# Kernel tuning notes

Measured on AMD Instinct MI355X. Metric: run time of the kernel, lower is better.

The kernel has to match this reference:

```python
import jax, jax.numpy as jnp
import numpy as np

NUM_USERS = 100000
NUM_ITEMS = 50000
EMB_DIM = 64
NNZ = 4800000
BATCH = 16384
N_LAYERS = 3


def setup_inputs() -> dict:
    key = jax.random.key(0)
    k0, k1, k2, k3, k4, k5 = jax.random.split(key, 6)
    N = NUM_USERS + NUM_ITEMS
    rows = jax.random.randint(k0, (NNZ,), 0, N, dtype=jnp.int32)
    cols = jax.random.randint(k1, (NNZ,), 0, N, dtype=jnp.int32)
    # symmetric normalization values: 1/sqrt(deg_out * deg_in), as in LightGCN preprocessing
    ones = jnp.ones((NNZ,), jnp.float32)
    deg_r = jax.ops.segment_sum(ones, rows, num_segments=N)
    deg_c = jax.ops.segment_sum(ones, cols, num_segments=N)
    vals = 1.0 / jnp.sqrt(jnp.maximum(deg_r[rows], 1.0) * jnp.maximum(deg_c[cols], 1.0))
    user_emb = 0.1 * jax.random.normal(k2, (NUM_USERS, EMB_DIM), jnp.float32)
    item_emb = 0.1 * jax.random.normal(k3, (NUM_ITEMS, EMB_DIM), jnp.float32)
    user_idx = jax.random.randint(k4, (BATCH,), 0, NUM_USERS, dtype=jnp.int64)
    item_idx = jax.random.randint(k5, (BATCH,), 0, NUM_ITEMS, dtype=jnp.int64)
    return {
        "user_emb": user_emb,
        "item_emb": item_emb,
        "rows": rows,
        "cols": cols,
        "vals": vals,
        "user_idx": user_idx,
        "item_idx": item_idx,
        "n_layers": N_LAYERS,
    }


def reference(user_emb, item_emb, rows, cols, vals, user_idx, item_idx, n_layers):
    num_users = user_emb.shape[0]
    N = num_users + item_emb.shape[0]
    all_emb = jnp.concatenate([user_emb, item_emb], axis=0)  # [N, D]
    acc = all_emb  # running sum over layer embeddings (embs[0] = E)
    emb = all_emb
    for _ in range(n_layers):
        # SpMM: out[r] = sum_{edges (r,c)} vals * emb[c]
        emb = jax.ops.segment_sum(vals[:, None] * emb[cols], rows, num_segments=N)
        acc = acc + emb
    light_out = acc / jnp.float32(n_layers + 1)  # mean over stacked layers
    u_e = light_out[user_idx]                     # [B, D]
    i_e = light_out[num_users + item_idx]         # [B, D]
    return (u_e * i_e).sum(axis=-1)               # [B]
```

## Files before the change

### kernel.cpp

```cpp
#include <hip/hip_runtime.h>
#include <hip/hip_fp16.h>

#define NUM_USERS 100000
#define NUM_ITEMS 50000
#define NN (NUM_USERS + NUM_ITEMS)
#define EMB_DIM 64
#define BATCH 16384
#define RPA 512
#define NBA ((NN + RPA - 1) / RPA)
#define SLOT 22528
#define NBLKA 768
#define CAP 16
#define OVF 32
#define SENT (1 << 27)
#define RSLOT 72

__device__ __forceinline__ unsigned h2u(__half2 h) {
    union { __half2 h; unsigned u; } x; x.h = h; return x.u;
}
__device__ __forceinline__ __half2 u2h(unsigned u) {
    union { __half2 h; unsigned u; } x; x.u = u; return x.h;
}

__global__ void lgcn_prep(unsigned long long* __restrict__ gq,
                          unsigned char* __restrict__ flags) {
    int i = blockIdx.x * blockDim.x + threadIdx.x;
    if (i < NBA) gq[i] = 0;
    for (int j = i; j < NN / 4; j += gridDim.x * blockDim.x)
        ((unsigned*)flags)[j] = 0;
    if (i == 0)
        for (int j = (NN / 4) * 4; j < NN; ++j) flags[j] = 0;
}

__global__ void __launch_bounds__(512) lgcn_binA(
        const float4* __restrict__ user_emb, const float4* __restrict__ item_emb,
        uint2* __restrict__ embh, int n_user4, int n_tot4,
        const int* __restrict__ rows, const int* __restrict__ cols,
        const float* __restrict__ vals, unsigned long long* __restrict__ gq,
        int2* __restrict__ cv_tmp, int nnz, int epb) {
    __shared__ int2 stage[CAP][NBA];
    __shared__ int  hist[NBA];
    __shared__ int  SBase[NBA];
    __shared__ int  pcnt[NBA];
    __shared__ int4 ovfBuf[2][OVF];
    __shared__ int  ovfCnt[2];
    int t = threadIdx.x;

    for (int i = blockIdx.x * 512 + t; i < n_tot4; i += NBLKA * 512) {
        float4 v = (i < n_user4) ? user_emb[i] : item_emb[i - n_user4];
        uint2 o;
        o.x = h2u(__float22half2_rn(make_float2(v.x, v.y)));
        o.y = h2u(__float22half2_rn(make_float2(v.z, v.w)));
        embh[i] = o;
    }

    int base = blockIdx.x * epb;
    int end  = base + epb; if (end > nnz) end = nnz;
    if (t < NBA) { hist[t] = 0; pcnt[t] = 0; }
    if (t == 0) { ovfCnt[0] = 0; ovfCnt[1] = 0; }
    __syncthreads();
    for (int i = base + t; i < end; i += 512)
        atomicAdd(&hist[rows[i] >> 9], 1);
    __syncthreads();
    if (t < NBA) {
        int c = hist[t];
        int p = 0;
        if (c) {
            int cp = (c + 7) & ~7;
            unsigned long long old = atomicAdd(&gq[t],
                ((unsigned long long)c << 32) | (unsigned)cp);
            p = (int)(unsigned)old;
        }
        SBase[t] = p;
    }
    __syncthreads();

    int p = 0;
    for (int r0 = base; r0 < end; r0 += 1024, p ^= 1) {
        int no = ovfCnt[p ^ 1];
        for (int j = t; j < no; j += 512) {
            int4 e = ovfBuf[p ^ 1][j];
            int b = e.w;
            int k = atomicAdd(&pcnt[b], 1);
            if (k < CAP) stage[k][b] = make_int2(e.x, e.y);
            else { int q = atomicAdd(&ovfCnt[p], 1);
                   if (q < OVF) ovfBuf[p][q] = e; }
        }
#pragma unroll
        for (int q2 = 0; q2 < 2; ++q2) {
            int i = r0 + q2 * 512 + t;
            if (i < end) {
                int r = rows[i];
                int b = r >> 9;
                __half hv = __float2half(vals[i]);
                int ex = ((r & 511) << 18) | cols[i];
                int ey = (int)h2u(__half2half2(hv));
                int k = atomicAdd(&pcnt[b], 1);
                if (k < CAP) stage[k][b] = make_int2(ex, ey);
                else { int q = atomicAdd(&ovfCnt[p], 1);
                       if (q < OVF) ovfBuf[p][q] = make_int4(ex, ey, 0, b); }
            }
        }
        __syncthreads();
        if (t < NBA) {
            int c = pcnt[t]; if (c > CAP) c = CAP;
            int g = c & ~7;
            if (g) {
                long long gb = (long long)t * SLOT + SBase[t];
                int4* dst = (int4*)&cv_tmp[gb];
                for (int j = 0; j < g; j += 2) {
                    int2 e0 = stage[j][t];
                    int2 e1 = stage[j + 1][t];
                    dst[j >> 1] = make_int4(e0.x, e0.y, e1.x, e1.y);
                }
                SBase[t] += g;
                for (int j = g; j < c; ++j) stage[j - g][t] = stage[j][t];
            }
            pcnt[t] = c - g;
        }
        if (t == 0) ovfCnt[p ^ 1] = 0;
        __syncthreads();
    }

    {
        int no = ovfCnt[p ^ 1];
        for (int j = t; j < no; j += 512) {
            int4 e = ovfBuf[p ^ 1][j];
            int b = e.w;
            int k = atomicAdd(&pcnt[b], 1);
            if (k < CAP) stage[k][b] = make_int2(e.x, e.y);
            else cv_tmp[(long long)b * SLOT + SBase[b] + k] =
                     make_int2(e.x, e.y);
        }
    }
    __syncthreads();
    if (t < NBA) {
        int c_raw = pcnt[t];
        int cl = min(c_raw, CAP);
        long long gb = (long long)t * SLOT + SBase[t];
        for (int j = 0; j < cl; ++j) cv_tmp[gb + j] = stage[j][t];
        int cp = (c_raw + 7) & ~7;
        for (int j = c_raw; j < cp; ++j) cv_tmp[gb + j] = make_int2(SENT, 0);
    }
}

__global__ void __launch_bounds__(1024) lgcn_binB(
        const unsigned long long* __restrict__ gq,
        const int2* __restrict__ cv_tmp, int2* __restrict__ cv,
        int* __restrict__ deg,
        const int* __restrict__ user_idx, const int* __restrict__ item_idx,
        unsigned char* __restrict__ flags) {
    __shared__ int cnt[RPA];
    int s = blockIdx.x;
    int t = threadIdx.x;
    long long w0 = (long long)s * SLOT;
    int wlen = (int)(unsigned)gq[s];
    int r0 = s * RPA;
    if (t < RPA) cnt[t] = 0;
    __syncthreads();
    for (int i = t; i < wlen; i += 1024) {
        int2 p = cv_tmp[w0 + i];
        int x = p.x;
        if (x & SENT) continue;
        int rl = (x >> 18) & 511;
        int pos = atomicAdd(&cnt[rl], 1);
        if (pos < RSLOT)
            cv[(long long)(r0 + rl) * RSLOT + pos] = p;
    }
    for (int i = s * 1024 + t; i < BATCH; i += NBA * 1024) {
        flags[user_idx[i]] = 1;
        flags[NUM_USERS + item_idx[i]] = 1;
    }
    __syncthreads();
    if (t < RPA) {
        int r = r0 + t;
        if (r < NN) deg[r] = min(cnt[t], RSLOT);
    }
}

__global__ void __launch_bounds__(256) lgcn_spmm(
        const int* __restrict__ deg,
        const int2* __restrict__ cv,
        const uint4* __restrict__ embh,
        uint4* __restrict__ nxth,
        const unsigned char* __restrict__ flags, int sel) {
    int wid = (blockIdx.x * blockDim.x + threadIdx.x) >> 6;
    int lane = threadIdx.x & 63;
    if (wid >= NN) return;
    if (sel && !flags[wid]) return;
    int n = deg[wid];
    int grp  = lane >> 3;
    int dim8 = lane & 7;
    const int2* ep = cv + (long long)wid * RSLOT;

    __half2 c0 = __float2half2_rn(0.f);
    __half2 c1 = c0, c2 = c0, c3 = c0;
    int m = n >> 3;
    int k = 0;
    for (; k + 4 <= m; k += 4) {
        int2 p[4]; uint4 raw[4];
#pragma unroll
        for (int j = 0; j < 4; ++j) p[j] = ep[8 * (k + j) + grp];
#pragma unroll
        for (int j = 0; j < 4; ++j)
            raw[j] = embh[(long long)(p[j].x & 0x3FFFF) * 8 + dim8];
#pragma unroll
        for (int j = 0; j < 4; ++j) {
            __half2 v2 = u2h((unsigned)p[j].y);
            c0 = __hfma2(v2, u2h(raw[j].x), c0);
            c1 = __hfma2(v2, u2h(raw[j].y), c1);
            c2 = __hfma2(v2, u2h(raw[j].z), c2);
            c3 = __hfma2(v2, u2h(raw[j].w), c3);
        }
    }
    for (; k + 2 <= m; k += 2) {
        int2 p[2]; uint4 raw[2];
#pragma unroll
        for (int j = 0; j < 2; ++j) p[j] = ep[8 * (k + j) + grp];
#pragma unroll
        for (int j = 0; j < 2; ++j)
            raw[j] = embh[(long long)(p[j].x & 0x3FFFF) * 8 + dim8];
#pragma unroll
        for (int j = 0; j < 2; ++j) {
            __half2 v2 = u2h((unsigned)p[j].y);
            c0 = __hfma2(v2, u2h(raw[j].x), c0);
            c1 = __hfma2(v2, u2h(raw[j].y), c1);
            c2 = __hfma2(v2, u2h(raw[j].z), c2);
            c3 = __hfma2(v2, u2h(raw[j].w), c3);
        }
    }
    for (; k < m; ++k) {
        int2 p = ep[8 * k + grp];
        uint4 raw = embh[(long long)(p.x & 0x3FFFF) * 8 + dim8];
        __half2 v2 = u2h((unsigned)p.y);
        c0 = __hfma2(v2, u2h(raw.x), c0);
        c1 = __hfma2(v2, u2h(raw.y), c1);
        c2 = __hfma2(v2, u2h(raw.z), c2);
        c3 = __hfma2(v2, u2h(raw.w), c3);
    }
    int rem = n & 7;
    if (grp < rem) {
        int2 p = ep[8 * m + grp];
        uint4 raw = embh[(long long)(p.x & 0x3FFFF) * 8 + dim8];
        __half2 v2 = u2h((unsigned)p.y);
        c0 = __hfma2(v2, u2h(raw.x), c0);
        c1 = __hfma2(v2, u2h(raw.y), c1);
        c2 = __hfma2(v2, u2h(raw.z), c2);
        c3 = __hfma2(v2, u2h(raw.w), c3);
    }

#pragma unroll
    for (int off = 8; off < 64; off <<= 1) {
        c0 = __hadd2(c0, u2h(__shfl_xor(h2u(c0), off)));
        c1 = __hadd2(c1, u2h(__shfl_xor(h2u(c1), off)));
        c2 = __hadd2(c2, u2h(__shfl_xor(h2u(c2), off)));
        c3 = __hadd2(c3, u2h(__shfl_xor(h2u(c3), off)));
    }
    if (grp == 0) {
        long long o = (long long)wid * 8 + dim8;
        uint4 ov;
        ov.x = h2u(c0); ov.y = h2u(c1); ov.z = h2u(c2); ov.w = h2u(c3);
        nxth[o] = ov;
    }
}

__global__ void lgcn_dot(const uint2* __restrict__ E0, const uint2* __restrict__ E1,
                         const uint2* __restrict__ E2, const uint2* __restrict__ E3,
                         const int* __restrict__ user_idx,
                         const int* __restrict__ item_idx,
                         float* __restrict__ out, int batch) {
    int t = blockIdx.x * blockDim.x + threadIdx.x;
    int b = t >> 4;
    if (b >= batch) return;
    int l = t & 15;
    long long ru = (long long)user_idx[b] * 16 + l;
    long long ri = (long long)(NUM_USERS + item_idx[b]) * 16 + l;
    float4 su = {0.f, 0.f, 0.f, 0.f};
    float4 si = {0.f, 0.f, 0.f, 0.f};
    const uint2* Es[4] = {E0, E1, E2, E3};
#pragma unroll
    for (int q = 0; q < 4; ++q) {
        uint2 a = Es[q][ru];
        uint2 c = Es[q][ri];
        float2 a0 = __half22float2(u2h(a.x)), a1 = __half22float2(u2h(a.y));
        float2 c0 = __half22float2(u2h(c.x)), c1 = __half22float2(u2h(c.y));
        su.x += a0.x; su.y += a0.y; su.z += a1.x; su.w += a1.y;
        si.x += c0.x; si.y += c0.y; si.z += c1.x; si.w += c1.y;
    }
    float s = su.x * si.x + su.y * si.y + su.z * si.z + su.w * si.w;
    s += __shfl_down(s, 8, 16);
    s += __shfl_down(s, 4, 16);
    s += __shfl_down(s, 2, 16);
    s += __shfl_down(s, 1, 16);
    if (l == 0) out[b] = s * (1.0f / 16.0f);
}

extern "C" void kernel_launch(void* const* d_in, const int* in_sizes, int n_in,
                              void* d_out, int out_size, void* d_ws, size_t ws_size,
                              hipStream_t stream) {
    const float* user_emb = (const float*)d_in[0];
    const float* item_emb = (const float*)d_in[1];
    const int*   rows     = (const int*)d_in[2];
    const int*   cols     = (const int*)d_in[3];
    const float* vals     = (const float*)d_in[4];
    const int*   user_idx = (const int*)d_in[5];
    const int*   item_idx = (const int*)d_in[6];
    float* out = (float*)d_out;

    const int nnz = in_sizes[2];
    const size_t node_uint2 = (size_t)NN * 16;

    uint2* E[4];
    E[0] = (uint2*)d_ws;
    E[1] = E[0] + node_uint2;
    E[2] = E[1] + node_uint2;
    E[3] = E[2] + node_uint2;
    int2*  cv      = (int2*)(E[3] + node_uint2);
    int*   deg     = (int*)(cv + (size_t)NN * RSLOT);
    unsigned long long* gq = (unsigned long long*)(deg + NN);
    unsigned char* flags = (unsigned char*)(gq + NBA);
    int2*  cv_tmp  = (int2*)E[1];

    const int n_tot4  = NN * EMB_DIM / 4;
    const int n_user4 = NUM_USERS * EMB_DIM / 4;
    const int epb = (nnz + NBLKA - 1) / NBLKA;

    lgcn_prep<<<64, 256, 0, stream>>>(gq, flags);

    lgcn_binA<<<NBLKA, 512, 0, stream>>>(
        (const float4*)user_emb, (const float4*)item_emb, E[0],
        n_user4, n_tot4, rows, cols, vals, gq, cv_tmp, nnz, epb);

    lgcn_binB<<<NBA, 1024, 0, stream>>>(gq, cv_tmp, cv, deg,
                                        user_idx, item_idx, flags);

    const int spmm_blocks = (NN * 64 + 255) / 256;
    for (int layer = 0; layer < 3; ++layer) {
        lgcn_spmm<<<spmm_blocks, 256, 0, stream>>>(deg, cv,
                                                   (const uint4*)E[layer],
                                                   (uint4*)E[layer + 1],
                                                   flags, layer == 2 ? 1 : 0);
    }

    lgcn_dot<<<(BATCH * 16 + 255) / 256, 256, 0, stream>>>(
        E[0], E[1], E[2], E[3], user_idx, item_idx, out, BATCH);
}
```

Measured before the change: 422.7 us.

## Pack edge column and quantized weight into one int, fuse layer sum into last SpMM

Edge records go from int2 (column plus half2 weight) to a single 32-bit word holding an 18-bit column and a 14-bit truncated fp16 weight. This halves the CSR-like edge stream read by each SpMM layer. The last SpMM layer now sums E0, E1, E2 and the new layer into an fp32 buffer for flagged nodes, so the dot kernel reads one buffer instead of four. binB is unrolled 4x for more loads in flight. The cost is reduced weight precision (low mantissa bits dropped) and a new fp32 sums workspace.

New measurement: 413.7 us. -2.1%, faster.

```diff
diff --git a/kernel.cpp b/kernel.cpp
--- a/kernel.cpp
+++ b/kernel.cpp
@@ -144,9 +144,15 @@
     }
 }
 
+#define BINB_PUT(p) do { int x = (p).x; if (!(x & SENT)) {                   \
+    int rl = (x >> 18) & 511; int pos = atomicAdd(&cnt[rl], 1);              \
+    if (pos < RSLOT) { int v16 = (p).y & 0xFFFF;                             \
+        cv[(long long)(r0 + rl) * RSLOT + pos] =                             \
+            (((v16 + 2) >> 2) << 18) | (x & 0x3FFFF); } } } while (0)
+
 __global__ void __launch_bounds__(1024) lgcn_binB(
         const unsigned long long* __restrict__ gq,
-        const int2* __restrict__ cv_tmp, int2* __restrict__ cv,
+        const int2* __restrict__ cv_tmp, int* __restrict__ cv,
         int* __restrict__ deg,
         const int* __restrict__ user_idx, const int* __restrict__ item_idx,
         unsigned char* __restrict__ flags) {
@@ -158,18 +164,21 @@
     int r0 = s * RPA;
     if (t < RPA) cnt[t] = 0;
     __syncthreads();
-    for (int i = t; i < wlen; i += 1024) {
+    int i = t;
+    for (; i + 3 * 1024 < wlen; i += 4096) {
+        int2 p0 = cv_tmp[w0 + i];
+        int2 p1 = cv_tmp[w0 + i + 1024];
+        int2 p2 = cv_tmp[w0 + i + 2048];
+        int2 p3 = cv_tmp[w0 + i + 3072];
+        BINB_PUT(p0); BINB_PUT(p1); BINB_PUT(p2); BINB_PUT(p3);
+    }
+    for (; i < wlen; i += 1024) {
         int2 p = cv_tmp[w0 + i];
-        int x = p.x;
-        if (x & SENT) continue;
-        int rl = (x >> 18) & 511;
-        int pos = atomicAdd(&cnt[rl], 1);
-        if (pos < RSLOT)
-            cv[(long long)(r0 + rl) * RSLOT + pos] = p;
-    }
-    for (int i = s * 1024 + t; i < BATCH; i += NBA * 1024) {
-        flags[user_idx[i]] = 1;
-        flags[NUM_USERS + item_idx[i]] = 1;
+        BINB_PUT(p);
+    }
+    for (int j = s * 1024 + t; j < BATCH; j += NBA * 1024) {
+        flags[user_idx[j]] = 1;
+        flags[NUM_USERS + item_idx[j]] = 1;
     }
     __syncthreads();
     if (t < RPA) {
@@ -180,10 +189,12 @@
 
 __global__ void __launch_bounds__(256) lgcn_spmm(
         const int* __restrict__ deg,
-        const int2* __restrict__ cv,
+        const int* __restrict__ cv,
         const uint4* __restrict__ embh,
         uint4* __restrict__ nxth,
-        const unsigned char* __restrict__ flags, int sel) {
+        const unsigned char* __restrict__ flags, int sel,
+        const uint4* __restrict__ e0t, const uint4* __restrict__ e1t,
+        float4* __restrict__ sums) {
     int wid = (blockIdx.x * blockDim.x + threadIdx.x) >> 6;
     int lane = threadIdx.x & 63;
     if (wid >= NN) return;
@@ -191,22 +202,23 @@
     int n = deg[wid];
     int grp  = lane >> 3;
     int dim8 = lane & 7;
-    const int2* ep = cv + (long long)wid * RSLOT;
+    const int* ep = cv + (long long)wid * RSLOT;
 
     __half2 c0 = __float2half2_rn(0.f);
     __half2 c1 = c0, c2 = c0, c3 = c0;
     int m = n >> 3;
     int k = 0;
     for (; k + 4 <= m; k += 4) {
-        int2 p[4]; uint4 raw[4];
+        int p[4]; uint4 raw[4];
 #pragma unroll
         for (int j = 0; j < 4; ++j) p[j] = ep[8 * (k + j) + grp];
 #pragma unroll
         for (int j = 0; j < 4; ++j)
-            raw[j] = embh[(long long)(p[j].x & 0x3FFFF) * 8 + dim8];
+            raw[j] = embh[(long long)(p[j] & 0x3FFFF) * 8 + dim8];
 #pragma unroll
         for (int j = 0; j < 4; ++j) {
-            __half2 v2 = u2h((unsigned)p[j].y);
+            unsigned vv = ((unsigned)p[j] >> 18) << 2;
+            __half2 v2 = u2h(vv | (vv << 16));
             c0 = __hfma2(v2, u2h(raw[j].x), c0);
             c1 = __hfma2(v2, u2h(raw[j].y), c1);
             c2 = __hfma2(v2, u2h(raw[j].z), c2);
@@ -214,15 +226,16 @@
         }
     }
     for (; k + 2 <= m; k += 2) {
-        int2 p[2]; uint4 raw[2];
+        int p[2]; uint4 raw[2];
 #pragma unroll
         for (int j = 0; j < 2; ++j) p[j] = ep[8 * (k + j) + grp];
 #pragma unroll
         for (int j = 0; j < 2; ++j)
-            raw[j] = embh[(long long)(p[j].x & 0x3FFFF) * 8 + dim8];
+            raw[j] = embh[(long long)(p[j] & 0x3FFFF) * 8 + dim8];
 #pragma unroll
         for (int j = 0; j < 2; ++j) {
-            __half2 v2 = u2h((unsigned)p[j].y);
+            unsigned vv = ((unsigned)p[j] >> 18) << 2;
+            __half2 v2 = u2h(vv | (vv << 16));
             c0 = __hfma2(v2, u2h(raw[j].x), c0);
             c1 = __hfma2(v2, u2h(raw[j].y), c1);
             c2 = __hfma2(v2, u2h(raw[j].z), c2);
@@ -230,9 +243,10 @@
         }
     }
     for (; k < m; ++k) {
-        int2 p = ep[8 * k + grp];
-        uint4 raw = embh[(long long)(p.x & 0x3FFFF) * 8 + dim8];
-        __half2 v2 = u2h((unsigned)p.y);
+        int p = ep[8 * k + grp];
+        uint4 raw = embh[(long long)(p & 0x3FFFF) * 8 + dim8];
+        unsigned vv = ((unsigned)p >> 18) << 2;
+        __half2 v2 = u2h(vv | (vv << 16));
         c0 = __hfma2(v2, u2h(raw.x), c0);
         c1 = __hfma2(v2, u2h(raw.y), c1);
         c2 = __hfma2(v2, u2h(raw.z), c2);
@@ -240,9 +254,10 @@
     }
     int rem = n & 7;
     if (grp < rem) {
-        int2 p = ep[8 * m + grp];
-        uint4 raw = embh[(long long)(p.x & 0x3FFFF) * 8 + dim8];
-        __half2 v2 = u2h((unsigned)p.y);
+        int p = ep[8 * m + grp];
+        uint4 raw = embh[(long long)(p & 0x3FFFF) * 8 + dim8];
+        unsigned vv = ((unsigned)p >> 18) << 2;
+        __half2 v2 = u2h(vv | (vv << 16));
         c0 = __hfma2(v2, u2h(raw.x), c0);
         c1 = __hfma2(v2, u2h(raw.y), c1);
         c2 = __hfma2(v2, u2h(raw.z), c2);
@@ -258,14 +273,35 @@
     }
     if (grp == 0) {
         long long o = (long long)wid * 8 + dim8;
-        uint4 ov;
-        ov.x = h2u(c0); ov.y = h2u(c1); ov.z = h2u(c2); ov.w = h2u(c3);
-        nxth[o] = ov;
-    }
-}
-
-__global__ void lgcn_dot(const uint2* __restrict__ E0, const uint2* __restrict__ E1,
-                         const uint2* __restrict__ E2, const uint2* __restrict__ E3,
+        if (!sel) {
+            uint4 ov;
+            ov.x = h2u(c0); ov.y = h2u(c1); ov.z = h2u(c2); ov.w = h2u(c3);
+            nxth[o] = ov;
+        } else {
+            uint4 r0v = e0t[o], r1v = e1t[o], r2v = embh[o];
+            float2 f0 = __half22float2(c0), f1 = __half22float2(c1);
+            float2 f2 = __half22float2(c2), f3 = __half22float2(c3);
+            float2 a;
+            a = __half22float2(u2h(r0v.x)); f0.x += a.x; f0.y += a.y;
+            a = __half22float2(u2h(r1v.x)); f0.x += a.x; f0.y += a.y;
+            a = __half22float2(u2h(r2v.x)); f0.x += a.x; f0.y += a.y;
+            a = __half22float2(u2h(r0v.y)); f1.x += a.x; f1.y += a.y;
+            a = __half22float2(u2h(r1v.y)); f1.x += a.x; f1.y += a.y;
+            a = __half22float2(u2h(r2v.y)); f1.x += a.x; f1.y += a.y;
+            a = __half22float2(u2h(r0v.z)); f2.x += a.x; f2.y += a.y;
+            a = __half22float2(u2h(r1v.z)); f2.x += a.x; f2.y += a.y;
+            a = __half22float2(u2h(r2v.z)); f2.x += a.x; f2.y += a.y;
+            a = __half22float2(u2h(r0v.w)); f3.x += a.x; f3.y += a.y;
+            a = __half22float2(u2h(r1v.w)); f3.x += a.x; f3.y += a.y;
+            a = __half22float2(u2h(r2v.w)); f3.x += a.x; f3.y += a.y;
+            long long so = (long long)wid * 16 + dim8 * 2;
+            sums[so]     = make_float4(f0.x, f0.y, f1.x, f1.y);
+            sums[so + 1] = make_float4(f2.x, f2.y, f3.x, f3.y);
+        }
+    }
+}
+
+__global__ void lgcn_dot(const float4* __restrict__ sums,
                          const int* __restrict__ user_idx,
                          const int* __restrict__ item_idx,
                          float* __restrict__ out, int batch) {
@@ -273,20 +309,8 @@
     int b = t >> 4;
     if (b >= batch) return;
     int l = t & 15;
-    long long ru = (long long)user_idx[b] * 16 + l;
-    long long ri = (long long)(NUM_USERS + item_idx[b]) * 16 + l;
-    float4 su = {0.f, 0.f, 0.f, 0.f};
-    float4 si = {0.f, 0.f, 0.f, 0.f};
-    const uint2* Es[4] = {E0, E1, E2, E3};
-#pragma unroll
-    for (int q = 0; q < 4; ++q) {
-        uint2 a = Es[q][ru];
-        uint2 c = Es[q][ri];
-        float2 a0 = __half22float2(u2h(a.x)), a1 = __half22float2(u2h(a.y));
-        float2 c0 = __half22float2(u2h(c.x)), c1 = __half22float2(u2h(c.y));
-        su.x += a0.x; su.y += a0.y; su.z += a1.x; su.w += a1.y;
-        si.x += c0.x; si.y += c0.y; si.z += c1.x; si.w += c1.y;
-    }
+    float4 su = sums[(long long)user_idx[b] * 16 + l];
+    float4 si = sums[(long long)(NUM_USERS + item_idx[b]) * 16 + l];
     float s = su.x * si.x + su.y * si.y + su.z * si.z + su.w * si.w;
     s += __shfl_down(s, 8, 16);
     s += __shfl_down(s, 4, 16);
@@ -315,11 +339,12 @@
     E[1] = E[0] + node_uint2;
     E[2] = E[1] + node_uint2;
     E[3] = E[2] + node_uint2;
-    int2*  cv      = (int2*)(E[3] + node_uint2);
-    int*   deg     = (int*)(cv + (size_t)NN * RSLOT);
+    int*    cv   = (int*)(E[3] + node_uint2);
+    float4* sums = (float4*)(cv + (size_t)NN * RSLOT);
+    int*    deg  = (int*)(sums + (size_t)NN * 16);
     unsigned long long* gq = (unsigned long long*)(deg + NN);
     unsigned char* flags = (unsigned char*)(gq + NBA);
-    int2*  cv_tmp  = (int2*)E[1];
+    int2*   cv_tmp = (int2*)E[1];
 
     const int n_tot4  = NN * EMB_DIM / 4;
     const int n_user4 = NUM_USERS * EMB_DIM / 4;
@@ -339,9 +364,11 @@
         lgcn_spmm<<<spmm_blocks, 256, 0, stream>>>(deg, cv,
                                                    (const uint4*)E[layer],
                                                    (uint4*)E[layer + 1],
-                                                   flags, layer == 2 ? 1 : 0);
+                                                   flags, layer == 2 ? 1 : 0,
+                                                   (const uint4*)E[0],
+                                                   (const uint4*)E[1], sums);
     }
 
     lgcn_dot<<<(BATCH * 16 + 255) / 256, 256, 0, stream>>>(
-        E[0], E[1], E[2], E[3], user_idx, item_idx, out, BATCH);
-}
+        sums, user_idx, item_idx, out, BATCH);
+}
```
